# Performance work log

Hardware: AMD Instinct MI355X
Metric: run time of the kernel (lower is better)

The kernel has to match this reference:

```python
import jax, jax.numpy as jnp
import numpy as np

N_CLASSES = 128
N_SUPPORT = 5
N_QUERIES = 15  # 20 - n_support, per the hard-coded 20 in the source
D_FEAT = 8192
K = 20
EPS = float(np.finfo(np.float64).eps)  # np.finfo(float).eps in source


def setup_inputs() -> dict:
    key = jax.random.key(0)
    k1, k2, k3 = jax.random.split(key, 3)
    N = N_CLASSES * (N_SUPPORT + N_QUERIES)
    feats = jax.random.normal(k1, (N, D_FEAT), dtype=jnp.float32)  # sigma-normalized pooled embeddings
    s_labels_idx = jax.random.randint(k2, (N_CLASSES * N_SUPPORT,), 0, N_CLASSES, dtype=jnp.int32)
    q_labels_idx = jax.random.randint(k3, (N_CLASSES * N_QUERIES,), 0, N_CLASSES, dtype=jnp.int32)
    alpha = jnp.ones((1,), dtype=jnp.float32) * 0.99
    return {"feats": feats, "alpha": alpha, "s_labels_idx": s_labels_idx,
            "q_labels_idx": q_labels_idx, "k": K}


def reference(feats, alpha, s_labels_idx, q_labels_idx, k):
    N, d = feats.shape
    # W[i,j] = exp(-mean((f_i - f_j)^2) / 2), computed via GEMM expansion
    sq = jnp.sum(feats * feats, axis=1)                      # [N]
    dist = (sq[:, None] + sq[None, :] - 2.0 * feats @ feats.T) / d
    W = jnp.exp(-dist / 2.0)                                 # [N, N]
    # top-k per row, scatter-mask, symmetrize (mask + mask.T > 0)
    _, idx = jax.lax.top_k(W, k)                             # [N, k]
    mask = jnp.zeros_like(W).at[jnp.arange(N)[:, None], idx].set(1.0)
    mask = ((mask + mask.T) > 0).astype(jnp.float32)
    W = W * mask
    # symmetric degree normalization S = D^-1/2 W D^-1/2
    D = W.sum(0)
    dsi = jnp.sqrt(1.0 / (D + EPS))
    S = dsi[:, None] * W * dsi[None, :]
    # closed-form label propagation: F = (I - alpha*S + eps)^-1 @ y
    ys = jax.nn.one_hot(s_labels_idx, N_CLASSES, dtype=jnp.float32)
    yu = jnp.zeros((N_CLASSES * N_QUERIES, N_CLASSES), dtype=jnp.float32)
    y = jnp.concatenate([ys, yu], axis=0)                    # [N, C]
    A = jnp.eye(N, dtype=jnp.float32) - alpha[0] * S + EPS   # scalar eps broadcast, as in source
    F_ = jnp.linalg.inv(A) @ y                               # [N, C]
    # cross-entropy over all rows with ground-truth class indices
    gt = jnp.concatenate([s_labels_idx, q_labels_idx], axis=0)
    logp = jax.nn.log_softmax(F_, axis=1)
    loss = -jnp.mean(jnp.take_along_axis(logp, gt[:, None].astype(jnp.int32), axis=1))
    # query accuracy
    Fq = F_[N_CLASSES * N_SUPPORT:, :]
    acc = jnp.mean((jnp.argmax(Fq, axis=1) == q_labels_idx).astype(jnp.float32))
    return loss, acc
```

## Files before the change

kernel.cpp:

```cpp
#include <hip/hip_runtime.h>
#include <hip/hip_fp8.h>
#include <stdint.h>

#define N 2560
#define NSUP 640
#define NQ 1920
#define NCLS 128
#define DF 8192
#define CAP 1024
#define TITER 8
#define EPSF 2.220446049250313e-16f

typedef __attribute__((ext_vector_type(4))) float f32x4;

__device__ __forceinline__ unsigned short f2bf(float f) {
  unsigned u = __float_as_uint(f);
  return (unsigned short)((u + 0x7FFFu + ((u >> 16) & 1u)) >> 16);
}
__device__ __forceinline__ float bf2f(unsigned short h) {
  return __uint_as_float(((unsigned)h) << 16);
}
__device__ __forceinline__ unsigned char f2e4m3(float f) {
  __hip_fp8_e4m3 h(f);
  return (unsigned char)h.__x;
}
__device__ __forceinline__ unsigned sortkey(float f) {
  unsigned u = __float_as_uint(f);
  return (u & 0x80000000u) ? ~u : (u | 0x80000000u);
}
__device__ __forceinline__ void load_lds16(const void* g, void* l) {
  __builtin_amdgcn_global_load_lds((const __attribute__((address_space(1))) void*)g,
                                   (__attribute__((address_space(3))) void*)l, 16, 0, 0);
}

__global__ void k_prep(const float* __restrict__ feats, unsigned char* __restrict__ fb8,
                       float* __restrict__ sq, const float* __restrict__ alpha,
                       float* __restrict__ rho_tab) {
  int i = blockIdx.x, t = threadIdx.x;
  const float4* src = (const float4*)(feats + (size_t)i * DF);
  uchar4* dst = (uchar4*)(fb8 + (size_t)i * DF);
  float s = 0.f;
#pragma unroll
  for (int it = 0; it < 8; ++it) {
    float4 v = src[it * 256 + t];
    s = fmaf(v.x, v.x, s); s = fmaf(v.y, v.y, s);
    s = fmaf(v.z, v.z, s); s = fmaf(v.w, v.w, s);
    uchar4 o; o.x = f2e4m3(v.x); o.y = f2e4m3(v.y); o.z = f2e4m3(v.z); o.w = f2e4m3(v.w);
    dst[it * 256 + t] = o;
  }
  __shared__ float red[256];
  red[t] = s; __syncthreads();
  for (int o = 128; o > 0; o >>= 1) { if (t < o) red[t] += red[t + o]; __syncthreads(); }
  if (t == 0) sq[i] = red[0];
  if (i == 0 && t == 0) {
    float a = alpha[0];
    float rho = a; rho_tab[0] = rho;
    for (int k2 = 1; k2 < 128; ++k2) { rho = 1.f / (2.f / a - rho); rho_tab[k2] = rho; }
  }
}

__global__ __launch_bounds__(256, 2) void k_gemm(const unsigned char* __restrict__ fb8,
                                                 unsigned short* __restrict__ C0,
                                                 unsigned short* __restrict__ C1,
                                                 unsigned short* __restrict__ C2) {
  __shared__ __align__(16) unsigned char As[128 * 64];
  __shared__ __align__(16) unsigned char Bs[128 * 64];
  int bid = blockIdx.x;
  int ks = (bid >= 210) + (bid >= 420);
  int tid2 = bid - 210 * ks;
  unsigned short* Cd = (ks == 0) ? C0 : (ks == 1 ? C1 : C2);
  const int kbase = ks * 2752;
  const int kend = kbase + (ks < 2 ? 2752 : 2688);
  int bx = (int)((sqrtf(8.0f * (float)tid2 + 1.0f) - 1.0f) * 0.5f);
  while ((bx + 1) * (bx + 2) / 2 <= tid2) ++bx;
  while (bx * (bx + 1) / 2 > tid2) --bx;
  int by = tid2 - bx * (bx + 1) / 2;
  const int rA = by * 128, rB = bx * 128;
  const int t = threadIdx.x, w = t >> 6, l = t & 63;
  const int q = l >> 4, m = l & 15;
  const int wr = w >> 1, wc = w & 1;
  f32x4 acc[4][4];
#pragma unroll
  for (int a2 = 0; a2 < 4; ++a2)
#pragma unroll
    for (int b2 = 0; b2 < 4; ++b2) acc[a2][b2] = (f32x4){0.f, 0.f, 0.f, 0.f};

  const int u0 = (w * 2 + 0) * 64 + l;
  const int u1 = (w * 2 + 1) * 64 + l;
  const int row0 = (u0 >> 1) & 127;
  const int ko0 = ((u0 >> 8) << 5) + ((((u0 & 1) ^ ((u0 >> 3) & 1))) << 4);
  const int row1 = (u1 >> 1) & 127;
  const int ko1 = ((u1 >> 8) << 5) + ((((u1 & 1) ^ ((u1 >> 3) & 1))) << 4);
  char* lA0 = (char*)As + (w * 2 + 0) * 1024;
  char* lA1 = (char*)As + (w * 2 + 1) * 1024;
  char* lB0 = (char*)Bs + (w * 2 + 0) * 1024;
  char* lB1 = (char*)Bs + (w * 2 + 1) * 1024;
  const int qoff = ((((q >> 1) ^ ((m >> 2) & 1))) << 4) + ((q & 1) << 3);

  for (int k0 = kbase; k0 < kend; k0 += 64) {
    load_lds16(fb8 + (size_t)(rA + row0) * DF + k0 + ko0, lA0);
    load_lds16(fb8 + (size_t)(rA + row1) * DF + k0 + ko1, lA1);
    load_lds16(fb8 + (size_t)(rB + row0) * DF + k0 + ko0, lB0);
    load_lds16(fb8 + (size_t)(rB + row1) * DF + k0 + ko1, lB1);
    asm volatile("s_waitcnt vmcnt(0)" ::: "memory");
    __syncthreads();
#pragma unroll
    for (int s2 = 0; s2 < 2; ++s2) {
      long long af[4], bv[4];
#pragma unroll
      for (int im = 0; im < 4; ++im)
        af[im] = *(const long long*)(As + s2 * 4096 + (wr * 64 + im * 16 + m) * 32 + qoff);
#pragma unroll
      for (int in = 0; in < 4; ++in)
        bv[in] = *(const long long*)(Bs + s2 * 4096 + (wc * 64 + in * 16 + m) * 32 + qoff);
#pragma unroll
      for (int im = 0; im < 4; ++im)
#pragma unroll
        for (int in = 0; in < 4; ++in)
          acc[im][in] = __builtin_amdgcn_mfma_f32_16x16x32_fp8_fp8(
              (long)af[im], (long)bv[in], acc[im][in], 0, 0, 0);
    }
    __syncthreads();
  }
#pragma unroll
  for (int im = 0; im < 4; ++im) {
    int row0w = rA + wr * 64 + im * 16 + q * 4;
#pragma unroll
    for (int in = 0; in < 4; ++in) {
      int col = rB + wc * 64 + in * 16 + m;
#pragma unroll
      for (int rg = 0; rg < 4; ++rg) {
        unsigned short h = f2bf(acc[im][in][rg]);
        Cd[(size_t)(row0w + rg) * N + col] = h;
        Cd[(size_t)col * N + row0w + rg] = h;
      }
    }
  }
}

__global__ void k_topk(const unsigned short* __restrict__ C0,
                       const unsigned short* __restrict__ C1,
                       const unsigned short* __restrict__ C2,
                       const float* __restrict__ sq, unsigned* __restrict__ M) {
  int i = blockIdx.x * 4 + (threadIdx.x >> 6);
  int lane = threadIdx.x & 63;
  const unsigned short* r0 = C0 + (size_t)i * N;
  const unsigned short* r1 = C1 + (size_t)i * N;
  const unsigned short* r2 = C2 + (size_t)i * N;
  unsigned kk[40];
#pragma unroll
  for (int s = 0; s < 40; ++s) {
    int j = lane + (s << 6);
    float c = bf2f(r0[j]) + bf2f(r1[j]) + bf2f(r2[j]);
    kk[s] = sortkey(2.f * c - sq[j]);
  }
  unsigned long long removed = 0ull;
  unsigned myj = 0u;
  for (int t = 0; t < 20; ++t) {
    unsigned bk = 0u; int bs = -1;
#pragma unroll
    for (int s = 0; s < 40; ++s)
      if (!((removed >> s) & 1ull) && kk[s] > bk) { bk = kk[s]; bs = s; }
    unsigned long long packed = (bs < 0) ? 0ull
        : ((((unsigned long long)bk) << 32) |
           (unsigned long long)(0xFFFFFFFFu - (unsigned)(lane + (bs << 6))));
#pragma unroll
    for (int off2 = 32; off2 > 0; off2 >>= 1) {
      unsigned long long o = __shfl_xor(packed, off2, 64);
      if (o > packed) packed = o;
    }
    unsigned jw = 0xFFFFFFFFu - (unsigned)(packed & 0xFFFFFFFFull);
    if ((int)(jw & 63u) == lane) removed |= 1ull << (jw >> 6);
    if (t == lane) myj = jw;
  }
  if (lane < 20) atomicOr(&M[(size_t)i * 80 + (myj >> 5)], 1u << (myj & 31u));
}

__global__ void k_csr(const unsigned short* __restrict__ C0,
                      const unsigned short* __restrict__ C1,
                      const unsigned short* __restrict__ C2,
                      const float* __restrict__ sq,
                      const unsigned* __restrict__ M, unsigned* __restrict__ csrG,
                      int* __restrict__ degG, float* __restrict__ dsi) {
  int i = blockIdx.x, t = threadIdx.x;
  __shared__ unsigned Mrow[80];
  __shared__ int degs;
  __shared__ unsigned packs[CAP];
  __shared__ float red[256];
  if (t < 80) Mrow[t] = M[(size_t)i * 80 + t];
  if (t == 0) degs = 0;
  __syncthreads();
  const unsigned short* r0c = C0 + (size_t)i * N;
  const unsigned short* r1c = C1 + (size_t)i * N;
  const unsigned short* r2c = C2 + (size_t)i * N;
  float sqi = sq[i];
  int iw = i >> 5; unsigned ib = 1u << (i & 31);
  float dsum = 0.f;
#pragma unroll
  for (int s = 0; s < 10; ++s) {
    int j = t + (s << 8);
    unsigned mij = (Mrow[j >> 5] >> (j & 31)) & 1u;
    unsigned mji = M[(size_t)j * 80 + iw] & ib;
    if (mij | (mji != 0u)) {
      float c = bf2f(r0c[j]) + bf2f(r1c[j]) + bf2f(r2c[j]);
      float wv = expf((2.f * c - sqi - sq[j]) * (1.f / 16384.f));
      int sl = atomicAdd(&degs, 1);
      if (sl < CAP) packs[sl] = (((unsigned)f2bf(wv)) << 16) | (unsigned)j;
      dsum += wv;
    }
  }
  red[t] = dsum; __syncthreads();
  for (int o = 128; o > 0; o >>= 1) { if (t < o) red[t] += red[t + o]; __syncthreads(); }
  if (t == 0) {
    degG[i] = degs > CAP ? CAP : degs;
    dsi[i] = 1.f / sqrtf(red[0] + EPSF);
  }
  __syncthreads();
  int dgc = degs > CAP ? CAP : degs;
  for (int sl = t; sl < dgc; sl += 256)
    csrG[(size_t)i * CAP + sl] = packs[sl];
}

__global__ void k_scale_init(unsigned* __restrict__ csrG, const int* __restrict__ degG,
                             const float* __restrict__ dsi, const int* __restrict__ slab,
                             float* __restrict__ x, float* __restrict__ r,
                             unsigned short* __restrict__ d0) {
  int i = blockIdx.x * 4 + (threadIdx.x >> 6);
  int lane = threadIdx.x & 63;
  float di = dsi[i];
  int dg = degG[i];
  for (int s = lane; s < dg; s += 64) {
    unsigned p = csrG[(size_t)i * CAP + s];
    int j = p & 0xFFFFu;
    float wv = __uint_as_float(p & 0xFFFF0000u);
    wv *= di * dsi[j];
    csrG[(size_t)i * CAP + s] = (((unsigned)f2bf(wv)) << 16) | (unsigned)j;
  }
  int c0 = 2 * lane;
  float y0 = 0.f, y1 = 0.f;
  if (i < NSUP) {
    int lbl = slab[i];
    y0 = (lbl == c0) ? 1.f : 0.f;
    y1 = (lbl == c0 + 1) ? 1.f : 0.f;
  }
  size_t o = (size_t)i * NCLS + c0;
  x[o] = 0.f; x[o + 1] = 0.f;
  r[o] = y0;  r[o + 1] = y1;
  ushort2 dini; dini.x = f2bf(y0); dini.y = f2bf(y1);
  *(ushort2*)(d0 + o) = dini;
}

__global__ __launch_bounds__(256) void k_cheby(const unsigned* __restrict__ csrG,
                        const int* __restrict__ degG, const float* __restrict__ rho_tab,
                        const float* __restrict__ alpha, float* __restrict__ x,
                        float* __restrict__ r, const unsigned short* __restrict__ dcur,
                        unsigned short* __restrict__ dnxt, int it) {
  int i = blockIdx.x;
  int t = threadIdx.x;
  int g4 = (t & 31) << 2, p = t >> 5;
  __shared__ unsigned lcv[CAP];
  __shared__ float4 partial[256];
  int dg = degG[i];
  for (int s = t; s < dg; s += 256) lcv[s] = csrG[(size_t)i * CAP + s];
  __syncthreads();
  float4 acc = make_float4(0.f, 0.f, 0.f, 0.f);
  int s = p;
  for (; s + 56 < dg; s += 64) {
    unsigned uu[8]; ushort4 a[8];
#pragma unroll
    for (int u = 0; u < 8; ++u) {
      uu[u] = lcv[s + 8 * u];
      a[u] = *(const ushort4*)(dcur + (size_t)(uu[u] & 0xFFFFu) * NCLS + g4);
    }
#pragma unroll
    for (int u = 0; u < 8; ++u) {
      float v = __uint_as_float(uu[u] & 0xFFFF0000u);
      acc.x = fmaf(v, bf2f(a[u].x), acc.x);
      acc.y = fmaf(v, bf2f(a[u].y), acc.y);
      acc.z = fmaf(v, bf2f(a[u].z), acc.z);
      acc.w = fmaf(v, bf2f(a[u].w), acc.w);
    }
  }
  for (; s < dg; s += 8) {
    unsigned uu = lcv[s];
    ushort4 a = *(const ushort4*)(dcur + (size_t)(uu & 0xFFFFu) * NCLS + g4);
    float v = __uint_as_float(uu & 0xFFFF0000u);
    acc.x = fmaf(v, bf2f(a.x), acc.x); acc.y = fmaf(v, bf2f(a.y), acc.y);
    acc.z = fmaf(v, bf2f(a.z), acc.z); acc.w = fmaf(v, bf2f(a.w), acc.w);
  }
  partial[t] = acc;
  __syncthreads();
  for (int off = 128; off >= 32; off >>= 1) {
    if (t < off) {
      float4 o = partial[t + off];
      float4 m = partial[t];
      m.x += o.x; m.y += o.y; m.z += o.z; m.w += o.w;
      partial[t] = m;
    }
    __syncthreads();
  }
  if (t < 32) {
    float4 ax = partial[t];
    float ahat = alpha[0];
    float rho = rho_tab[it], rhon = rho_tab[it + 1];
    float cc1 = rhon * rho, cc2 = 2.f * rhon / ahat;
    size_t o = (size_t)i * NCLS + 4 * t;
    ushort4 dv = *(const ushort4*)(dcur + o);
    float4 di; di.x = bf2f(dv.x); di.y = bf2f(dv.y); di.z = bf2f(dv.z); di.w = bf2f(dv.w);
    float4 xv = *(float4*)(x + o);
    float4 rv = *(float4*)(r + o);
    float4 q;
    q.x = di.x - ahat * ax.x; q.y = di.y - ahat * ax.y;
    q.z = di.z - ahat * ax.z; q.w = di.w - ahat * ax.w;
    xv.x += di.x; xv.y += di.y; xv.z += di.z; xv.w += di.w;
    rv.x -= q.x; rv.y -= q.y; rv.z -= q.z; rv.w -= q.w;
    ushort4 dn;
    dn.x = f2bf(cc1 * di.x + cc2 * rv.x); dn.y = f2bf(cc1 * di.y + cc2 * rv.y);
    dn.z = f2bf(cc1 * di.z + cc2 * rv.z); dn.w = f2bf(cc1 * di.w + cc2 * rv.w);
    *(float4*)(x + o) = xv;
    *(float4*)(r + o) = rv;
    *(ushort4*)(dnxt + o) = dn;
  }
}

__global__ void k_loss(const float* __restrict__ F, const int* __restrict__ slab,
                       const int* __restrict__ qlab, float* __restrict__ lossSum,
                       int* __restrict__ accCnt) {
  int i = blockIdx.x * 4 + (threadIdx.x >> 6);
  int lane = threadIdx.x & 63;
  int c0 = 2 * lane;
  float2 f = *(const float2*)(F + (size_t)i * NCLS + c0);
  float mx = fmaxf(f.x, f.y);
  for (int o2 = 32; o2 > 0; o2 >>= 1) mx = fmaxf(mx, __shfl_xor(mx, o2, 64));
  float se = expf(f.x - mx) + expf(f.y - mx);
  for (int o2 = 32; o2 > 0; o2 >>= 1) se += __shfl_xor(se, o2, 64);
  float lse = mx + logf(se);
  int gt = (i < NSUP) ? slab[i] : qlab[i - NSUP];
  float fg = ((c0 == gt) ? f.x : 0.f) + ((c0 + 1 == gt) ? f.y : 0.f);
  for (int o2 = 32; o2 > 0; o2 >>= 1) fg += __shfl_xor(fg, o2, 64);
  if (lane == 0) atomicAdd(lossSum, fg - lse);
  if (i >= NSUP) {
    float bvv; int bc;
    if (f.y > f.x) { bvv = f.y; bc = c0 + 1; } else { bvv = f.x; bc = c0; }
    unsigned long long packed =
        (((unsigned long long)sortkey(bvv)) << 32) | (unsigned long long)(unsigned)(127 - bc);
    for (int o2 = 32; o2 > 0; o2 >>= 1) {
      unsigned long long o = __shfl_xor(packed, o2, 64);
      if (o > packed) packed = o;
    }
    int cw = 127 - (int)(packed & 0xFFFFFFFFull);
    if (lane == 0 && cw == qlab[i - NSUP]) atomicAdd(accCnt, 1);
  }
}

__global__ void k_final(const float* __restrict__ lossSum, const int* __restrict__ accCnt,
                        float* __restrict__ out) {
  out[0] = -lossSum[0] / (float)N;
  out[1] = (float)accCnt[0] / (float)NQ;
}

extern "C" void kernel_launch(void* const* d_in, const int* in_sizes, int n_in,
                              void* d_out, int out_size, void* d_ws, size_t ws_size,
                              hipStream_t stream) {
  const float* feats = (const float*)d_in[0];
  const float* alpha = (const float*)d_in[1];
  const int* slab = (const int*)d_in[2];
  const int* qlab = (const int*)d_in[3];
  float* out = (float*)d_out;
  char* ws = (char*)d_ws;

  unsigned short* C0 = (unsigned short*)(ws + 0);
  unsigned short* C1 = (unsigned short*)(ws + 13107200);
  unsigned short* C2 = (unsigned short*)(ws + 26214400);
  float* x           = (float*)(ws + 0);
  float* r           = (float*)(ws + 1310720);
  unsigned short* d0 = (unsigned short*)(ws + 2621440);
  unsigned short* d1 = (unsigned short*)(ws + 3276800);
  unsigned* M   = (unsigned*)(ws + 39321600);
  float* ctrl   = (float*)(ws + 40140800);
  float* lossSum = ctrl;
  int* accCnt   = (int*)(ctrl + 1);
  float* rho_tab = ctrl + 4;
  float* sq     = (float*)(ws + 40141824);
  float* dsi    = (float*)(ws + 40152064);
  int* degG     = (int*)(ws + 40162304);
  unsigned char* fb8 = (unsigned char*)(ws + 40172544);
  unsigned* csrG = (unsigned*)(ws + 40172544);

  hipMemsetAsync(ws + 39321600, 0, 820224, stream);
  k_prep<<<N, 256, 0, stream>>>(feats, fb8, sq, alpha, rho_tab);
  k_gemm<<<630, 256, 0, stream>>>(fb8, C0, C1, C2);
  k_topk<<<N / 4, 256, 0, stream>>>(C0, C1, C2, sq, M);
  k_csr<<<N, 256, 0, stream>>>(C0, C1, C2, sq, M, csrG, degG, dsi);
  k_scale_init<<<N / 4, 256, 0, stream>>>(csrG, degG, dsi, slab, x, r, d0);
  for (int it = 0; it < TITER; ++it) {
    const unsigned short* dc = (it & 1) ? d1 : d0;
    unsigned short* dn = (it & 1) ? d0 : d1;
    k_cheby<<<N, 256, 0, stream>>>(csrG, degG, rho_tab, alpha, x, r, dc, dn, it);
  }
  k_loss<<<N / 4, 256, 0, stream>>>(x, slab, qlab, lossSum, accCnt);
  k_final<<<1, 1, 0, stream>>>(lossSum, accCnt, out);
}
```

Before: 401.9 us.

## Map one wavefront per row in Chebyshev SpMM, drop LDS reduction

Restructures the Chebyshev iteration kernel so that each 64-lane wavefront handles a whole row, with lanes covering 2 classes each. Neighbour indices are broadcast with shuffles instead of being staged through shared memory, which removes the cross-block partial-sum reduction and all __syncthreads. Each block now processes four rows. In exchange, each wavefront walks all neighbours serially, so there is less memory-level parallelism per row, and gathers shrink from 8-byte to 4-byte loads.

```diff
diff --git a/kernel.cpp b/kernel.cpp
--- a/kernel.cpp
+++ b/kernel.cpp
@@ -255,72 +255,55 @@
                         const float* __restrict__ alpha, float* __restrict__ x,
                         float* __restrict__ r, const unsigned short* __restrict__ dcur,
                         unsigned short* __restrict__ dnxt, int it) {
-  int i = blockIdx.x;
-  int t = threadIdx.x;
-  int g4 = (t & 31) << 2, p = t >> 5;
-  __shared__ unsigned lcv[CAP];
-  __shared__ float4 partial[256];
+  int i = blockIdx.x * 4 + (threadIdx.x >> 6);
+  int l = threadIdx.x & 63;
   int dg = degG[i];
-  for (int s = t; s < dg; s += 256) lcv[s] = csrG[(size_t)i * CAP + s];
-  __syncthreads();
-  float4 acc = make_float4(0.f, 0.f, 0.f, 0.f);
-  int s = p;
-  for (; s + 56 < dg; s += 64) {
-    unsigned uu[8]; ushort4 a[8];
-#pragma unroll
-    for (int u = 0; u < 8; ++u) {
-      uu[u] = lcv[s + 8 * u];
-      a[u] = *(const ushort4*)(dcur + (size_t)(uu[u] & 0xFFFFu) * NCLS + g4);
-    }
-#pragma unroll
-    for (int u = 0; u < 8; ++u) {
-      float v = __uint_as_float(uu[u] & 0xFFFF0000u);
-      acc.x = fmaf(v, bf2f(a[u].x), acc.x);
-      acc.y = fmaf(v, bf2f(a[u].y), acc.y);
-      acc.z = fmaf(v, bf2f(a[u].z), acc.z);
-      acc.w = fmaf(v, bf2f(a[u].w), acc.w);
-    }
-  }
-  for (; s < dg; s += 8) {
-    unsigned uu = lcv[s];
-    ushort4 a = *(const ushort4*)(dcur + (size_t)(uu & 0xFFFFu) * NCLS + g4);
-    float v = __uint_as_float(uu & 0xFFFF0000u);
-    acc.x = fmaf(v, bf2f(a.x), acc.x); acc.y = fmaf(v, bf2f(a.y), acc.y);
-    acc.z = fmaf(v, bf2f(a.z), acc.z); acc.w = fmaf(v, bf2f(a.w), acc.w);
-  }
-  partial[t] = acc;
-  __syncthreads();
-  for (int off = 128; off >= 32; off >>= 1) {
-    if (t < off) {
-      float4 o = partial[t + off];
-      float4 m = partial[t];
-      m.x += o.x; m.y += o.y; m.z += o.z; m.w += o.w;
-      partial[t] = m;
-    }
-    __syncthreads();
-  }
-  if (t < 32) {
-    float4 ax = partial[t];
-    float ahat = alpha[0];
-    float rho = rho_tab[it], rhon = rho_tab[it + 1];
-    float cc1 = rhon * rho, cc2 = 2.f * rhon / ahat;
-    size_t o = (size_t)i * NCLS + 4 * t;
-    ushort4 dv = *(const ushort4*)(dcur + o);
-    float4 di; di.x = bf2f(dv.x); di.y = bf2f(dv.y); di.z = bf2f(dv.z); di.w = bf2f(dv.w);
-    float4 xv = *(float4*)(x + o);
-    float4 rv = *(float4*)(r + o);
-    float4 q;
-    q.x = di.x - ahat * ax.x; q.y = di.y - ahat * ax.y;
-    q.z = di.z - ahat * ax.z; q.w = di.w - ahat * ax.w;
-    xv.x += di.x; xv.y += di.y; xv.z += di.z; xv.w += di.w;
-    rv.x -= q.x; rv.y -= q.y; rv.z -= q.z; rv.w -= q.w;
-    ushort4 dn;
-    dn.x = f2bf(cc1 * di.x + cc2 * rv.x); dn.y = f2bf(cc1 * di.y + cc2 * rv.y);
-    dn.z = f2bf(cc1 * di.z + cc2 * rv.z); dn.w = f2bf(cc1 * di.w + cc2 * rv.w);
-    *(float4*)(x + o) = xv;
-    *(float4*)(r + o) = rv;
-    *(ushort4*)(dnxt + o) = dn;
-  }
+  const unsigned* crow = csrG + (size_t)i * CAP;
+  float accx = 0.f, accy = 0.f;
+  for (int base = 0; base < dg; base += 64) {
+    int idx = base + l;
+    unsigned pv = (idx < dg) ? crow[idx] : 0u;
+    int nrem = dg - base; if (nrem > 64) nrem = 64;
+    int s = 0;
+    for (; s + 8 <= nrem; s += 8) {
+      unsigned pp[8]; ushort2 aa[8];
+#pragma unroll
+      for (int u = 0; u < 8; ++u) pp[u] = __shfl(pv, s + u, 64);
+#pragma unroll
+      for (int u = 0; u < 8; ++u)
+        aa[u] = *(const ushort2*)(dcur + (size_t)(pp[u] & 0xFFFFu) * NCLS + 2 * l);
+#pragma unroll
+      for (int u = 0; u < 8; ++u) {
+        float v = __uint_as_float(pp[u] & 0xFFFF0000u);
+        accx = fmaf(v, bf2f(aa[u].x), accx);
+        accy = fmaf(v, bf2f(aa[u].y), accy);
+      }
+    }
+    for (; s < nrem; ++s) {
+      unsigned p = __shfl(pv, s, 64);
+      ushort2 a = *(const ushort2*)(dcur + (size_t)(p & 0xFFFFu) * NCLS + 2 * l);
+      float v = __uint_as_float(p & 0xFFFF0000u);
+      accx = fmaf(v, bf2f(a.x), accx);
+      accy = fmaf(v, bf2f(a.y), accy);
+    }
+  }
+  float ahat = alpha[0];
+  float rho = rho_tab[it], rhon = rho_tab[it + 1];
+  float cc1 = rhon * rho, cc2 = 2.f * rhon / ahat;
+  size_t o = (size_t)i * NCLS + 2 * l;
+  ushort2 dv = *(const ushort2*)(dcur + o);
+  float dix = bf2f(dv.x), diy = bf2f(dv.y);
+  float2 xv = *(float2*)(x + o);
+  float2 rv = *(float2*)(r + o);
+  float qx = dix - ahat * accx, qy = diy - ahat * accy;
+  xv.x += dix; xv.y += diy;
+  rv.x -= qx;  rv.y -= qy;
+  ushort2 dn;
+  dn.x = f2bf(cc1 * dix + cc2 * rv.x);
+  dn.y = f2bf(cc1 * diy + cc2 * rv.y);
+  *(float2*)(x + o) = xv;
+  *(float2*)(r + o) = rv;
+  *(ushort2*)(dnxt + o) = dn;
 }
 
 __global__ void k_loss(const float* __restrict__ F, const int* __restrict__ slab,
@@ -396,7 +379,7 @@
   for (int it = 0; it < TITER; ++it) {
     const unsigned short* dc = (it & 1) ? d1 : d0;
     unsigned short* dn = (it & 1) ? d0 : d1;
-    k_cheby<<<N, 256, 0, stream>>>(csrG, degG, rho_tab, alpha, x, r, dc, dn, it);
+    k_cheby<<<N / 4, 256, 0, stream>>>(csrG, degG, rho_tab, alpha, x, r, dc, dn, it);
   }
   k_loss<<<N / 4, 256, 0, stream>>>(x, slab, qlab, lossSum, accCnt);
   k_final<<<1, 1, 0, stream>>>(lossSum, accCnt, out);
```

Result: slower. 676.4 us (+68.3%).

## Double-buffer GEMM LDS tiles and build transposed top-k mask for CSR

Applied to the files above, without the earlier changes.

The fp8 GEMM now keeps two LDS buffers and issues the next k-slice's global-to-LDS loads before computing on the current one, so load latency can overlap with MFMA work. k_topk also writes a transposed mask MT with atomics, which lets k_csr read the symmetric neighbour bits from one contiguous row instead of doing strided per-element reads of M. The cost is double the GEMM shared memory, which may reduce occupancy, plus an extra memset and more atomics in the top-k step.

```diff
diff --git a/kernel.cpp b/kernel.cpp
--- a/kernel.cpp
+++ b/kernel.cpp
@@ -63,8 +63,8 @@
                                                  unsigned short* __restrict__ C0,
                                                  unsigned short* __restrict__ C1,
                                                  unsigned short* __restrict__ C2) {
-  __shared__ __align__(16) unsigned char As[128 * 64];
-  __shared__ __align__(16) unsigned char Bs[128 * 64];
+  __shared__ __align__(16) unsigned char As[2][128 * 64];
+  __shared__ __align__(16) unsigned char Bs[2][128 * 64];
   int bid = blockIdx.x;
   int ks = (bid >= 210) + (bid >= 420);
   int tid2 = bid - 210 * ks;
@@ -91,28 +91,40 @@
   const int ko0 = ((u0 >> 8) << 5) + ((((u0 & 1) ^ ((u0 >> 3) & 1))) << 4);
   const int row1 = (u1 >> 1) & 127;
   const int ko1 = ((u1 >> 8) << 5) + ((((u1 & 1) ^ ((u1 >> 3) & 1))) << 4);
-  char* lA0 = (char*)As + (w * 2 + 0) * 1024;
-  char* lA1 = (char*)As + (w * 2 + 1) * 1024;
-  char* lB0 = (char*)Bs + (w * 2 + 0) * 1024;
-  char* lB1 = (char*)Bs + (w * 2 + 1) * 1024;
+  const int so0 = (w * 2 + 0) * 1024;
+  const int so1 = (w * 2 + 1) * 1024;
   const int qoff = ((((q >> 1) ^ ((m >> 2) & 1))) << 4) + ((q & 1) << 3);
 
+  const size_t gA0 = (size_t)(rA + row0) * DF + ko0;
+  const size_t gA1 = (size_t)(rA + row1) * DF + ko1;
+  const size_t gB0 = (size_t)(rB + row0) * DF + ko0;
+  const size_t gB1 = (size_t)(rB + row1) * DF + ko1;
+
+#define STAGE(K0, BUF)                                                  \
+  do {                                                                  \
+    load_lds16(fb8 + gA0 + (K0), (char*)As[BUF] + so0);                 \
+    load_lds16(fb8 + gA1 + (K0), (char*)As[BUF] + so1);                 \
+    load_lds16(fb8 + gB0 + (K0), (char*)Bs[BUF] + so0);                 \
+    load_lds16(fb8 + gB1 + (K0), (char*)Bs[BUF] + so1);                 \
+  } while (0)
+
+  STAGE(kbase, 0);
+  asm volatile("s_waitcnt vmcnt(0)" ::: "memory");
+  __syncthreads();
+  int cur = 0;
   for (int k0 = kbase; k0 < kend; k0 += 64) {
-    load_lds16(fb8 + (size_t)(rA + row0) * DF + k0 + ko0, lA0);
-    load_lds16(fb8 + (size_t)(rA + row1) * DF + k0 + ko1, lA1);
-    load_lds16(fb8 + (size_t)(rB + row0) * DF + k0 + ko0, lB0);
-    load_lds16(fb8 + (size_t)(rB + row1) * DF + k0 + ko1, lB1);
-    asm volatile("s_waitcnt vmcnt(0)" ::: "memory");
-    __syncthreads();
+    if (k0 + 64 < kend) STAGE(k0 + 64, cur ^ 1);
+    const unsigned char* Ab = As[cur];
+    const unsigned char* Bb = Bs[cur];
 #pragma unroll
     for (int s2 = 0; s2 < 2; ++s2) {
       long long af[4], bv[4];
 #pragma unroll
       for (int im = 0; im < 4; ++im)
-        af[im] = *(const long long*)(As + s2 * 4096 + (wr * 64 + im * 16 + m) * 32 + qoff);
+        af[im] = *(const long long*)(Ab + s2 * 4096 + (wr * 64 + im * 16 + m) * 32 + qoff);
 #pragma unroll
       for (int in = 0; in < 4; ++in)
-        bv[in] = *(const long long*)(Bs + s2 * 4096 + (wc * 64 + in * 16 + m) * 32 + qoff);
+        bv[in] = *(const long long*)(Bb + s2 * 4096 + (wc * 64 + in * 16 + m) * 32 + qoff);
 #pragma unroll
       for (int im = 0; im < 4; ++im)
 #pragma unroll
@@ -120,8 +132,11 @@
           acc[im][in] = __builtin_amdgcn_mfma_f32_16x16x32_fp8_fp8(
               (long)af[im], (long)bv[in], acc[im][in], 0, 0, 0);
     }
+    asm volatile("s_waitcnt vmcnt(0)" ::: "memory");
     __syncthreads();
-  }
+    cur ^= 1;
+  }
+#undef STAGE
 #pragma unroll
   for (int im = 0; im < 4; ++im) {
     int row0w = rA + wr * 64 + im * 16 + q * 4;
@@ -141,7 +156,8 @@
 __global__ void k_topk(const unsigned short* __restrict__ C0,
                        const unsigned short* __restrict__ C1,
                        const unsigned short* __restrict__ C2,
-                       const float* __restrict__ sq, unsigned* __restrict__ M) {
+                       const float* __restrict__ sq, unsigned* __restrict__ M,
+                       unsigned* __restrict__ MT) {
   int i = blockIdx.x * 4 + (threadIdx.x >> 6);
   int lane = threadIdx.x & 63;
   const unsigned short* r0 = C0 + (size_t)i * N;
@@ -173,35 +189,39 @@
     if ((int)(jw & 63u) == lane) removed |= 1ull << (jw >> 6);
     if (t == lane) myj = jw;
   }
-  if (lane < 20) atomicOr(&M[(size_t)i * 80 + (myj >> 5)], 1u << (myj & 31u));
+  if (lane < 20) {
+    atomicOr(&M[(size_t)i * 80 + (myj >> 5)], 1u << (myj & 31u));
+    atomicOr(&MT[(size_t)myj * 80 + (i >> 5)], 1u << (i & 31u));
+  }
 }
 
 __global__ void k_csr(const unsigned short* __restrict__ C0,
                       const unsigned short* __restrict__ C1,
                       const unsigned short* __restrict__ C2,
                       const float* __restrict__ sq,
-                      const unsigned* __restrict__ M, unsigned* __restrict__ csrG,
+                      const unsigned* __restrict__ M, const unsigned* __restrict__ MT,
+                      unsigned* __restrict__ csrG,
                       int* __restrict__ degG, float* __restrict__ dsi) {
   int i = blockIdx.x, t = threadIdx.x;
   __shared__ unsigned Mrow[80];
+  __shared__ unsigned MTrow[80];
   __shared__ int degs;
   __shared__ unsigned packs[CAP];
   __shared__ float red[256];
   if (t < 80) Mrow[t] = M[(size_t)i * 80 + t];
+  if (t >= 128 && t < 208) MTrow[t - 128] = MT[(size_t)i * 80 + (t - 128)];
   if (t == 0) degs = 0;
   __syncthreads();
   const unsigned short* r0c = C0 + (size_t)i * N;
   const unsigned short* r1c = C1 + (size_t)i * N;
   const unsigned short* r2c = C2 + (size_t)i * N;
   float sqi = sq[i];
-  int iw = i >> 5; unsigned ib = 1u << (i & 31);
   float dsum = 0.f;
 #pragma unroll
   for (int s = 0; s < 10; ++s) {
     int j = t + (s << 8);
-    unsigned mij = (Mrow[j >> 5] >> (j & 31)) & 1u;
-    unsigned mji = M[(size_t)j * 80 + iw] & ib;
-    if (mij | (mji != 0u)) {
+    unsigned mm = (Mrow[j >> 5] | MTrow[j >> 5]) >> (j & 31);
+    if (mm & 1u) {
       float c = bf2f(r0c[j]) + bf2f(r1c[j]) + bf2f(r2c[j]);
       float wv = expf((2.f * c - sqi - sq[j]) * (1.f / 16384.f));
       int sl = atomicAdd(&degs, 1);
@@ -386,12 +406,14 @@
   int* degG     = (int*)(ws + 40162304);
   unsigned char* fb8 = (unsigned char*)(ws + 40172544);
   unsigned* csrG = (unsigned*)(ws + 40172544);
+  unsigned* MT  = (unsigned*)(ws + 50658304);
 
   hipMemsetAsync(ws + 39321600, 0, 820224, stream);
   k_prep<<<N, 256, 0, stream>>>(feats, fb8, sq, alpha, rho_tab);
   k_gemm<<<630, 256, 0, stream>>>(fb8, C0, C1, C2);
-  k_topk<<<N / 4, 256, 0, stream>>>(C0, C1, C2, sq, M);
-  k_csr<<<N, 256, 0, stream>>>(C0, C1, C2, sq, M, csrG, degG, dsi);
+  hipMemsetAsync(ws + 50658304, 0, 819200, stream);
+  k_topk<<<N / 4, 256, 0, stream>>>(C0, C1, C2, sq, M, MT);
+  k_csr<<<N, 256, 0, stream>>>(C0, C1, C2, sq, M, MT, csrG, degG, dsi);
   k_scale_init<<<N / 4, 256, 0, stream>>>(csrG, degG, dsi, slab, x, r, d0);
   for (int it = 0; it < TITER; ++it) {
     const unsigned short* dc = (it & 1) ? d1 : d0;
```

Result: faster. 382.7 us (-4.8%).
